# Kernel optimization log

Measured on AMD Instinct MI355X. Metric: run time of the kernel, lower is better.

Reference implementation:

```python
import jax, jax.numpy as jnp
import numpy as np


def _safe_pow(v, p):
    # mimic torch.nan_to_num(pow(v, p), nan=0, posinf=0, neginf=0) for v >= 0
    out = jnp.where(v > 0, jnp.power(jnp.where(v > 0, v, 1.0), p), 0.0)
    return out.astype(jnp.float32)


def setup_inputs() -> dict:
    key = jax.random.key(0)
    k1, k2, k3 = jax.random.split(key, 3)
    N, E, Din, Dout = 20000, 4096, 128, 128
    x = jax.random.normal(k1, (N, Din), dtype=jnp.float32)
    H = jax.random.uniform(k2, (N, E), dtype=jnp.float32)
    W = jax.random.normal(k3, (Dout, Din), dtype=jnp.float32) * (1.0 / np.sqrt(Din))
    b = jnp.zeros((Dout,), dtype=jnp.float32)
    return {"x": x, "H": H, "W": W, "b": b}


def reference(x, H, W, b):
    # Dv^{-1/2}: node degrees; De^{-1}: hyperedge degrees.
    # torch.diag(...)**p with nan/inf->0 is exactly diagonal scaling, so we
    # use broadcasted vector scaling fused around the two GEMMs.
    dv = _safe_pow(jnp.sum(H, axis=-1), -0.5)   # [N]
    de = _safe_pow(jnp.sum(H, axis=0), -1.0)    # [E]
    x = dv[:, None] * x                          # Dv^{-1/2} x
    x = H.T @ x                                  # [E, Din]
    x = de[:, None] * x                          # De^{-1}
    x = H @ x                                    # [N, Din]
    x = dv[:, None] * x                          # Dv^{-1/2}
    return x @ W.T + b                           # Linear
```

## Files before the change

kernel.cpp:

```cpp
#include <hip/hip_runtime.h>
#include <hip/hip_bf16.h>
#include <stdint.h>


#define N_ 20000
#define E_ 4096
#define D_ 128
#define XTB_S 20032
#define SPLIT 12

typedef __attribute__((ext_vector_type(8))) short    bf16x8;
typedef __attribute__((ext_vector_type(4))) float    f32x4;
typedef __attribute__((ext_vector_type(8))) unsigned short us8;
typedef __attribute__((ext_vector_type(4))) unsigned short us4;

__device__ __forceinline__ unsigned short f2bf(float f) {
  unsigned u = __float_as_uint(f);
  u += 0x7FFFu + ((u >> 16) & 1u);
  return (unsigned short)(u >> 16);
}
__device__ __forceinline__ unsigned cvtpk(float lo, float hi) {
  unsigned r;
  asm("v_cvt_pk_bf16_f32 %0, %1, %2" : "=v"(r) : "v"(lo), "v"(hi));
  return r;
}
__device__ __forceinline__ void gload16(const unsigned short* g, unsigned short* l) {
  __builtin_amdgcn_global_load_lds(
      (const __attribute__((address_space(1))) unsigned int*)g,
      (__attribute__((address_space(3))) unsigned int*)l, 16, 0, 0);
}

__global__ __launch_bounds__(256) void k_pre(const float* __restrict__ H,
                                             const float* __restrict__ x,
                                             const float* __restrict__ W,
                                             float* __restrict__ dv,
                                             unsigned short* __restrict__ Hb,
                                             unsigned short* __restrict__ xTb,
                                             unsigned short* __restrict__ Wb) {
  const int t = threadIdx.x, lane = t & 63, w = t >> 6;
  const int b = blockIdx.x;
  if (b >= 2500) {
    const size_t base = (size_t)(20000 + (b - 2500) * 8) * E_;
    for (int i = t; i < 4096; i += 256)
      *(us8*)&Hb[base + (size_t)i * 8] = (us8){0,0,0,0,0,0,0,0};
    if (b == 2500 && t < 128) {
#pragma unroll
      for (int c = 0; c < 4; ++c)
        *(us8*)&xTb[(size_t)t * XTB_S + 20000 + c * 8] = (us8){0,0,0,0,0,0,0,0};
    }
    if (b == 2501) {
      int base2 = t * 64;
#pragma unroll
      for (int i = 0; i < 8; ++i) {
        const float* wp = W + base2 + i * 8;
        f32x4 a = *(const f32x4*)wp, b4 = *(const f32x4*)(wp + 4);
        union { us8 v; unsigned u[4]; } un;
        un.u[0] = cvtpk(a.x, a.y);   un.u[1] = cvtpk(a.z, a.w);
        un.u[2] = cvtpk(b4.x, b4.y); un.u[3] = cvtpk(b4.z, b4.w);
        *(us8*)(Wb + base2 + i * 8) = un.v;
      }
    }
    return;
  }
  __shared__ float red[32];
  __shared__ float xt[8 * 128];
  const int n0 = b * 8;
  { int r = t >> 5, d4 = (t & 31) * 4;
    *(f32x4*)&xt[r * 128 + d4] = *(const f32x4*)(x + (size_t)(n0 + r) * D_ + d4); }
  float rs[8];
#pragma unroll
  for (int r = 0; r < 8; ++r) {
    rs[r] = 0.f;
    const float* rp = H + (size_t)(n0 + r) * E_;
    unsigned short* hp = Hb + (size_t)(n0 + r) * E_;
#pragma unroll
    for (int j = 0; j < 4; ++j) {
      f32x4 v = *(const f32x4*)(rp + j * 1024 + t * 4);
      rs[r] += (v.x + v.y) + (v.z + v.w);
      union { us4 v4; unsigned u32[2]; } un;
      un.u32[0] = cvtpk(v.x, v.y);
      un.u32[1] = cvtpk(v.z, v.w);
      *(us4*)(hp + j * 1024 + t * 4) = un.v4;
    }
  }
#pragma unroll
  for (int r = 0; r < 8; ++r)
#pragma unroll
    for (int off = 32; off; off >>= 1) rs[r] += __shfl_xor(rs[r], off);
  if (lane == 0) {
#pragma unroll
    for (int r = 0; r < 8; ++r) red[w * 8 + r] = rs[r];
  }
  __syncthreads();
  if (t < 8) {
    float s = red[t] + red[8 + t] + red[16 + t] + red[24 + t];
    float d = s > 0.f ? rsqrtf(s) : 0.f;
    dv[n0 + t] = d;
    red[t] = d;
  }
  __syncthreads();
  if (t < 128) {
    int d = t;
    float v[8];
#pragma unroll
    for (int r = 0; r < 8; ++r) v[r] = xt[r * 128 + d] * red[r];
    union { us8 v8; unsigned u32[4]; } un;
#pragma unroll
    for (int j = 0; j < 4; ++j) un.u32[j] = cvtpk(v[2 * j], v[2 * j + 1]);
    *(us8*)(xTb + (size_t)d * XTB_S + n0) = un.v8;
  }
}

__global__ __launch_bounds__(256) void k_gemm1(const unsigned short* __restrict__ Hb,
                                               const unsigned short* __restrict__ xTb,
                                               float* __restrict__ partialT,
                                               float* __restrict__ desumP) {
  __shared__ unsigned short lH[2][64 * 64];
  __shared__ unsigned short lX[2][128 * 64];
  const int t = threadIdx.x, lane = t & 63, w = t >> 6;
  const int eb = blockIdx.x & 63, s = blockIdx.x >> 6;
  const int e0 = eb * 64;
  const int g0 = (s * 313) / SPLIT;
  const int g1 = ((s + 1) * 313) / SPLIT;
  const int lrow = lane >> 3, lslot = lane & 7;
  const int bswz = (lslot ^ lrow) << 3;
  const int wy = w >> 1, wx = w & 1;
  const int ep = t & 31, q = t >> 5;
  const int er0 = 2 * ep, er1 = 2 * ep + 1;
  const int sl0 = (q ^ (er0 & 7)) << 3, sl1 = (q ^ (er1 & 7)) << 3;

  f32x4 acc[4][2];
  f32x4 accC[2];
#pragma unroll
  for (int i = 0; i < 4; ++i)
#pragma unroll
    for (int j = 0; j < 2; ++j) acc[i][j] = (f32x4){0.f, 0.f, 0.f, 0.f};
  accC[0] = (f32x4){0.f, 0.f, 0.f, 0.f};
  accC[1] = (f32x4){0.f, 0.f, 0.f, 0.f};
  bf16x8 ones;
#pragma unroll
  for (int i = 0; i < 8; ++i) ones[i] = (short)0x3F80;

  unsigned hr[8];
  auto LOADH = [&](int g) {
    const unsigned short* p = Hb + (size_t)(g * 64 + q * 8) * E_ + e0 + er0;
#pragma unroll
    for (int j = 0; j < 8; ++j) hr[j] = *(const unsigned*)(p + (size_t)j * E_);
  };
  auto WRITEH = [&](int bufi) {
    union { bf16x8 v; unsigned u[4]; } lo, hi;
#pragma unroll
    for (int p = 0; p < 4; ++p) {
      lo.u[p] = (hr[2 * p] & 0xFFFFu) | (hr[2 * p + 1] << 16);
      hi.u[p] = (hr[2 * p] >> 16) | (hr[2 * p + 1] & 0xFFFF0000u);
    }
    *(bf16x8*)&lH[bufi][er0 * 64 + sl0] = lo.v;
    *(bf16x8*)&lH[bufi][er1 * 64 + sl1] = hi.v;
  };
  auto GLOADX = [&](int g, int bufi) {
#pragma unroll
    for (int i = 0; i < 4; ++i) {
      int c = w * 4 + i;
      gload16(xTb + (size_t)(8 * c + lrow) * XTB_S + g * 64 + bswz,
              &lX[bufi][c * 512]);
    }
  };

  LOADH(g0); GLOADX(g0, 0); WRITEH(0);
  __syncthreads();
  int cur = 0;
  for (int it = g0; it < g1; ++it) {
    bool hn = it + 1 < g1;
    if (hn) { LOADH(it + 1); GLOADX(it + 1, cur ^ 1); }
    const int kg = lane >> 4, fr = lane & 15;
    bf16x8 ax[4][2], bh[2][2];
#pragma unroll
    for (int mi = 0; mi < 4; ++mi) {
      int m = wy * 64 + mi * 16 + fr;
#pragma unroll
      for (int kk = 0; kk < 2; ++kk)
        ax[mi][kk] = *(const bf16x8*)&lX[cur][m * 64 + (((kk * 4 + kg) ^ (m & 7)) << 3)];
    }
#pragma unroll
    for (int ni = 0; ni < 2; ++ni) {
      int n = wx * 32 + ni * 16 + fr;
#pragma unroll
      for (int kk = 0; kk < 2; ++kk)
        bh[ni][kk] = *(const bf16x8*)&lH[cur][n * 64 + (((kk * 4 + kg) ^ (n & 7)) << 3)];
    }
#pragma unroll
    for (int kk = 0; kk < 2; ++kk)
#pragma unroll
      for (int mi = 0; mi < 4; ++mi)
#pragma unroll
        for (int ni = 0; ni < 2; ++ni)
          acc[mi][ni] = __builtin_amdgcn_mfma_f32_16x16x32_bf16(ax[mi][kk], bh[ni][kk], acc[mi][ni], 0, 0, 0);
    if (wy == 0) {
#pragma unroll
      for (int kk = 0; kk < 2; ++kk)
#pragma unroll
        for (int ni = 0; ni < 2; ++ni)
          accC[ni] = __builtin_amdgcn_mfma_f32_16x16x32_bf16(ones, bh[ni][kk], accC[ni], 0, 0, 0);
    }
    if (hn) WRITEH(cur ^ 1);
    __syncthreads();
    cur ^= 1;
  }
  const int kg = lane >> 4, fr = lane & 15;
  if (wy == 0 && kg == 0) {
#pragma unroll
    for (int ni = 0; ni < 2; ++ni)
      desumP[s * E_ + e0 + wx * 32 + ni * 16 + fr] = accC[ni][0];
  }
#pragma unroll
  for (int mi = 0; mi < 4; ++mi)
#pragma unroll
    for (int ni = 0; ni < 2; ++ni)
#pragma unroll
      for (int r = 0; r < 4; ++r) {
        int d = wy * 64 + mi * 16 + kg * 4 + r;
        int e = e0 + wx * 32 + ni * 16 + fr;
        partialT[((size_t)s * 128 + d) * E_ + e] = acc[mi][ni][r];
      }
}

__global__ __launch_bounds__(256) void k_mid(const float* __restrict__ partialT,
                                             const float* __restrict__ desumP,
                                             const unsigned short* __restrict__ Wb,
                                             unsigned short* __restrict__ x3WT) {
  __shared__ unsigned short lW[128 * 136];
  __shared__ unsigned short lE[16 * 132];
  __shared__ float lT[128 * 20];
  const int t = threadIdx.x, lane = t & 63, w = t >> 6;
  const int e0 = blockIdx.x * 16;

  {
    int j = t >> 1, half = (t & 1) * 64;
    const us8* src = (const us8*)(Wb + (size_t)j * 128 + half);
#pragma unroll
    for (int i = 0; i < 8; ++i)
      *(us8*)&lW[j * 136 + half + 8 * i] = src[i];
  }
  {
    const int e = e0 + (t & 15);
    const int d0 = (t >> 4) * 8;
    float des = 0.f;
#pragma unroll
    for (int s = 0; s < SPLIT; ++s) des += desumP[s * E_ + e];
    float dei = des > 0.f ? 1.f / des : 0.f;
    float accp[8];
#pragma unroll
    for (int i = 0; i < 8; ++i) accp[i] = 0.f;
#pragma unroll
    for (int s = 0; s < SPLIT; ++s) {
      const float* p = partialT + ((size_t)s * 128 + d0) * E_ + e;
#pragma unroll
      for (int i = 0; i < 8; ++i) accp[i] += p[(size_t)i * E_];
    }
    union { bf16x8 v; unsigned u[4]; } un;
#pragma unroll
    for (int i = 0; i < 4; ++i)
      un.u[i] = cvtpk(accp[2 * i] * dei, accp[2 * i + 1] * dei);
    *(bf16x8*)&lE[(t & 15) * 132 + d0] = un.v;
  }
  __syncthreads();
  const int kg = lane >> 4, fr = lane & 15;
  f32x4 acc[2];
  acc[0] = (f32x4){0.f, 0.f, 0.f, 0.f};
  acc[1] = (f32x4){0.f, 0.f, 0.f, 0.f};
#pragma unroll
  for (int kk = 0; kk < 4; ++kk) {
    bf16x8 bfrag = *(const bf16x8*)&lE[fr * 132 + (kk * 4 + kg) * 8];
#pragma unroll
    for (int mi = 0; mi < 2; ++mi) {
      int m = w * 32 + mi * 16 + fr;
      bf16x8 afrag = *(const bf16x8*)&lW[m * 136 + (kk * 4 + kg) * 8];
      acc[mi] = __builtin_amdgcn_mfma_f32_16x16x32_bf16(afrag, bfrag, acc[mi], 0, 0, 0);
    }
  }
  __syncthreads();
#pragma unroll
  for (int mi = 0; mi < 2; ++mi)
#pragma unroll
    for (int r = 0; r < 4; ++r)
      lT[(w * 32 + mi * 16 + kg * 4 + r) * 20 + fr] = acc[mi][r];
  __syncthreads();
  {
    int j = t >> 1, eh = (t & 1) * 8;
    float v[8];
#pragma unroll
    for (int i = 0; i < 8; ++i) v[i] = lT[j * 20 + eh + i];
    union { us8 v8; unsigned u[4]; } un;
#pragma unroll
    for (int i = 0; i < 4; ++i) un.u[i] = cvtpk(v[2 * i], v[2 * i + 1]);
    *(us8*)(x3WT + (size_t)j * E_ + e0 + eh) = un.v8;
  }
}

__global__ __launch_bounds__(256) void k_gemm2(const unsigned short* __restrict__ Hb,
                                               const unsigned short* __restrict__ x3WT,
                                               const float* __restrict__ dv,
                                               const float* __restrict__ bias,
                                               float* __restrict__ out) {
  __shared__ unsigned short lA[2][64 * 64];
  __shared__ unsigned short lB[2][128 * 64];
  const int t = threadIdx.x, lane = t & 63, w = t >> 6;
  const int n0b = blockIdx.x * 64;
  const int lrow = lane >> 3, lslot = lane & 7;
  const int bswz = (lslot ^ lrow) << 3;
  const int wy = w >> 1, wx = w & 1;

  auto GLOADA = [&](int g, int bufi) {
#pragma unroll
    for (int i = 0; i < 2; ++i) {
      int c = w * 2 + i;
      gload16(Hb + (size_t)(n0b + 8 * c + lrow) * E_ + g * 64 + bswz,
              &lA[bufi][c * 512]);
    }
  };
  auto GLOADB = [&](int g, int bufi) {
#pragma unroll
    for (int i = 0; i < 4; ++i) {
      int c = w * 4 + i;
      gload16(x3WT + (size_t)(8 * c + lrow) * E_ + g * 64 + bswz,
              &lB[bufi][c * 512]);
    }
  };

  f32x4 acc[2][4];
#pragma unroll
  for (int i = 0; i < 2; ++i)
#pragma unroll
    for (int j = 0; j < 4; ++j) acc[i][j] = (f32x4){0.f, 0.f, 0.f, 0.f};

  GLOADA(0, 0); GLOADB(0, 0);
  __syncthreads();
  int cur = 0;
  for (int it = 0; it < 64; ++it) {
    bool hn = it < 63;
    if (hn) { GLOADA(it + 1, cur ^ 1); GLOADB(it + 1, cur ^ 1); }
    const int kg = lane >> 4, fr = lane & 15;
    bf16x8 af[2][2], bfr[4][2];
#pragma unroll
    for (int mi = 0; mi < 2; ++mi) {
      int m = wy * 32 + mi * 16 + fr;
#pragma unroll
      for (int kk = 0; kk < 2; ++kk)
        af[mi][kk] = *(const bf16x8*)&lA[cur][m * 64 + (((kk * 4 + kg) ^ (m & 7)) << 3)];
    }
#pragma unroll
    for (int ni = 0; ni < 4; ++ni) {
      int d = wx * 64 + ni * 16 + fr;
#pragma unroll
      for (int kk = 0; kk < 2; ++kk)
        bfr[ni][kk] = *(const bf16x8*)&lB[cur][d * 64 + (((kk * 4 + kg) ^ (d & 7)) << 3)];
    }
#pragma unroll
    for (int kk = 0; kk < 2; ++kk)
#pragma unroll
      for (int mi = 0; mi < 2; ++mi)
#pragma unroll
        for (int ni = 0; ni < 4; ++ni)
          acc[mi][ni] = __builtin_amdgcn_mfma_f32_16x16x32_bf16(af[mi][kk], bfr[ni][kk], acc[mi][ni], 0, 0, 0);
    __syncthreads();
    cur ^= 1;
  }
  const int kg = lane >> 4, fr = lane & 15;
#pragma unroll
  for (int mi = 0; mi < 2; ++mi) {
    float dvv[4];
#pragma unroll
    for (int r = 0; r < 4; ++r)
      dvv[r] = dv[min(n0b + wy * 32 + mi * 16 + kg * 4 + r, N_ - 1)];
#pragma unroll
    for (int ni = 0; ni < 4; ++ni) {
      int j2 = wx * 64 + ni * 16 + fr;
      float bb = bias[j2];
#pragma unroll
      for (int r = 0; r < 4; ++r) {
        int n = n0b + wy * 32 + mi * 16 + kg * 4 + r;
        if (n < N_) out[(size_t)n * D_ + j2] = acc[mi][ni][r] * dvv[r] + bb;
      }
    }
  }
}

extern "C" void kernel_launch(void* const* d_in, const int* in_sizes, int n_in,
                              void* d_out, int out_size, void* d_ws, size_t ws_size,
                              hipStream_t stream) {
  const float* x = (const float*)d_in[0];
  const float* H = (const float*)d_in[1];
  const float* W = (const float*)d_in[2];
  const float* b = (const float*)d_in[3];
  float* out = (float*)d_out;
  char* ws = (char*)d_ws;
  float*          desumP   = (float*)(ws);
  float*          dv       = (float*)(ws + 196608);
  unsigned short* Wb       = (unsigned short*)(ws + 276736);
  unsigned short* xTb      = (unsigned short*)(ws + 309504);
  unsigned short* x3WT     = (unsigned short*)(ws + 5437696);
  float*          partialT = (float*)(ws + 6486272);
  unsigned short* Hb       = (unsigned short*)(ws + 31652096);

  k_pre<<<2504, 256, 0, stream>>>(H, x, W, dv, Hb, xTb, Wb);
  k_gemm1<<<768, 256, 0, stream>>>(Hb, xTb, partialT, desumP);
  k_mid<<<256, 256, 0, stream>>>(partialT, desumP, Wb, x3WT);
  k_gemm2<<<313, 256, 0, stream>>>(Hb, x3WT, dv, b, out);
}
```

Baseline: 224.0 us.

## Triple-buffer LDS in both GEMMs with explicit vmcnt waits and reduce split

```diff
diff --git a/kernel.cpp b/kernel.cpp
--- a/kernel.cpp
+++ b/kernel.cpp
@@ -7,7 +7,7 @@
 #define E_ 4096
 #define D_ 128
 #define XTB_S 20032
-#define SPLIT 12
+#define SPLIT 8
 
 typedef __attribute__((ext_vector_type(8))) short    bf16x8;
 typedef __attribute__((ext_vector_type(4))) float    f32x4;
@@ -29,6 +29,9 @@
       (const __attribute__((address_space(1))) unsigned int*)g,
       (__attribute__((address_space(3))) unsigned int*)l, 16, 0, 0);
 }
+#define VMCNT(n) asm volatile("s_waitcnt vmcnt(" #n ")" ::: "memory")
+#define LGKM0()  asm volatile("s_waitcnt lgkmcnt(0)" ::: "memory")
+#define BAR()    do { __builtin_amdgcn_s_barrier(); __builtin_amdgcn_sched_barrier(0); } while (0)
 
 __global__ __launch_bounds__(256) void k_pre(const float* __restrict__ H,
                                              const float* __restrict__ x,
@@ -116,7 +119,7 @@
                                                float* __restrict__ partialT,
                                                float* __restrict__ desumP) {
   __shared__ unsigned short lH[2][64 * 64];
-  __shared__ unsigned short lX[2][128 * 64];
+  __shared__ unsigned short lX[3][128 * 64];
   const int t = threadIdx.x, lane = t & 63, w = t >> 6;
   const int eb = blockIdx.x & 63, s = blockIdx.x >> 6;
   const int e0 = eb * 64;
@@ -166,12 +169,20 @@
     }
   };
 
-  LOADH(g0); GLOADX(g0, 0); WRITEH(0);
-  __syncthreads();
-  int cur = 0;
+  LOADH(g0);
+  GLOADX(g0, 0);
+  GLOADX(g0 + 1, 1);
+  WRITEH(0);
+  VMCNT(4);
+  LGKM0();
+  BAR();
+
+  int cur = 0, curH = 0;
   for (int it = g0; it < g1; ++it) {
-    bool hn = it + 1 < g1;
-    if (hn) { LOADH(it + 1); GLOADX(it + 1, cur ^ 1); }
+    const bool hn = it + 1 < g1;
+    if (hn) LOADH(it + 1);
+    const int tn = (it + 2 < g1) ? it + 2 : g1 - 1;
+    GLOADX(tn, cur == 0 ? 2 : cur - 1);
     const int kg = lane >> 4, fr = lane & 15;
     bf16x8 ax[4][2], bh[2][2];
 #pragma unroll
@@ -186,8 +197,9 @@
       int n = wx * 32 + ni * 16 + fr;
 #pragma unroll
       for (int kk = 0; kk < 2; ++kk)
-        bh[ni][kk] = *(const bf16x8*)&lH[cur][n * 64 + (((kk * 4 + kg) ^ (n & 7)) << 3)];
-    }
+        bh[ni][kk] = *(const bf16x8*)&lH[curH][n * 64 + (((kk * 4 + kg) ^ (n & 7)) << 3)];
+    }
+    __builtin_amdgcn_s_setprio(1);
 #pragma unroll
     for (int kk = 0; kk < 2; ++kk)
 #pragma unroll
@@ -202,9 +214,13 @@
         for (int ni = 0; ni < 2; ++ni)
           accC[ni] = __builtin_amdgcn_mfma_f32_16x16x32_bf16(ones, bh[ni][kk], accC[ni], 0, 0, 0);
     }
-    if (hn) WRITEH(cur ^ 1);
-    __syncthreads();
-    cur ^= 1;
+    __builtin_amdgcn_s_setprio(0);
+    if (hn) WRITEH(curH ^ 1);
+    VMCNT(4);
+    LGKM0();
+    BAR();
+    cur = (cur == 2) ? 0 : cur + 1;
+    curH ^= 1;
   }
   const int kg = lane >> 4, fr = lane & 15;
   if (wy == 0 && kg == 0) {
@@ -302,23 +318,21 @@
                                                const float* __restrict__ dv,
                                                const float* __restrict__ bias,
                                                float* __restrict__ out) {
-  __shared__ unsigned short lA[2][64 * 64];
-  __shared__ unsigned short lB[2][128 * 64];
+  __shared__ unsigned short lA[3][64 * 64];
+  __shared__ unsigned short lB[3][128 * 64];
   const int t = threadIdx.x, lane = t & 63, w = t >> 6;
   const int n0b = blockIdx.x * 64;
   const int lrow = lane >> 3, lslot = lane & 7;
   const int bswz = (lslot ^ lrow) << 3;
   const int wy = w >> 1, wx = w & 1;
 
-  auto GLOADA = [&](int g, int bufi) {
+  auto STAGE = [&](int g, int bufi) {
 #pragma unroll
     for (int i = 0; i < 2; ++i) {
       int c = w * 2 + i;
       gload16(Hb + (size_t)(n0b + 8 * c + lrow) * E_ + g * 64 + bswz,
               &lA[bufi][c * 512]);
     }
-  };
-  auto GLOADB = [&](int g, int bufi) {
 #pragma unroll
     for (int i = 0; i < 4; ++i) {
       int c = w * 4 + i;
@@ -333,12 +347,15 @@
 #pragma unroll
     for (int j = 0; j < 4; ++j) acc[i][j] = (f32x4){0.f, 0.f, 0.f, 0.f};
 
-  GLOADA(0, 0); GLOADB(0, 0);
-  __syncthreads();
+  STAGE(0, 0);
+  STAGE(1, 1);
+  VMCNT(6);
+  BAR();
+
   int cur = 0;
   for (int it = 0; it < 64; ++it) {
-    bool hn = it < 63;
-    if (hn) { GLOADA(it + 1, cur ^ 1); GLOADB(it + 1, cur ^ 1); }
+    const int tn = (it + 2 < 64) ? it + 2 : 63;
+    STAGE(tn, cur == 0 ? 2 : cur - 1);
     const int kg = lane >> 4, fr = lane & 15;
     bf16x8 af[2][2], bfr[4][2];
 #pragma unroll
@@ -355,6 +372,7 @@
       for (int kk = 0; kk < 2; ++kk)
         bfr[ni][kk] = *(const bf16x8*)&lB[cur][d * 64 + (((kk * 4 + kg) ^ (d & 7)) << 3)];
     }
+    __builtin_amdgcn_s_setprio(1);
 #pragma unroll
     for (int kk = 0; kk < 2; ++kk)
 #pragma unroll
@@ -362,8 +380,10 @@
 #pragma unroll
         for (int ni = 0; ni < 4; ++ni)
           acc[mi][ni] = __builtin_amdgcn_mfma_f32_16x16x32_bf16(af[mi][kk], bfr[ni][kk], acc[mi][ni], 0, 0, 0);
-    __syncthreads();
-    cur ^= 1;
+    __builtin_amdgcn_s_setprio(0);
+    VMCNT(6);
+    BAR();
+    cur = (cur == 2) ? 0 : cur + 1;
   }
   const int kg = lane >> 4, fr = lane & 15;
 #pragma unroll
@@ -395,15 +415,15 @@
   float* out = (float*)d_out;
   char* ws = (char*)d_ws;
   float*          desumP   = (float*)(ws);
-  float*          dv       = (float*)(ws + 196608);
-  unsigned short* Wb       = (unsigned short*)(ws + 276736);
-  unsigned short* xTb      = (unsigned short*)(ws + 309504);
-  unsigned short* x3WT     = (unsigned short*)(ws + 5437696);
-  float*          partialT = (float*)(ws + 6486272);
-  unsigned short* Hb       = (unsigned short*)(ws + 31652096);
+  float*          dv       = (float*)(ws + 131072);
+  unsigned short* Wb       = (unsigned short*)(ws + 211200);
+  unsigned short* xTb      = (unsigned short*)(ws + 243968);
+  unsigned short* x3WT     = (unsigned short*)(ws + 5372160);
+  float*          partialT = (float*)(ws + 6420736);
+  unsigned short* Hb       = (unsigned short*)(ws + 23197952);
 
   k_pre<<<2504, 256, 0, stream>>>(H, x, W, dv, Hb, xTb, Wb);
-  k_gemm1<<<768, 256, 0, stream>>>(Hb, xTb, partialT, desumP);
+  k_gemm1<<<512, 256, 0, stream>>>(Hb, xTb, partialT, desumP);
   k_mid<<<256, 256, 0, stream>>>(partialT, desumP, Wb, x3WT);
   k_gemm2<<<313, 256, 0, stream>>>(Hb, x3WT, dv, b, out);
 }
```

Result: no change. 228.3 us (+1.9%).

## Split-K the second GEMM into two halves, add reduction kernel, remap gemm1 blocks

Applied to the files above, without the earlier changes.

```diff
diff --git a/kernel.cpp b/kernel.cpp
--- a/kernel.cpp
+++ b/kernel.cpp
@@ -118,7 +118,8 @@
   __shared__ unsigned short lH[2][64 * 64];
   __shared__ unsigned short lX[2][128 * 64];
   const int t = threadIdx.x, lane = t & 63, w = t >> 6;
-  const int eb = blockIdx.x & 63, s = blockIdx.x >> 6;
+  const int virt = (blockIdx.x & 7) * 96 + (blockIdx.x >> 3);
+  const int eb = virt & 63, s = virt >> 6;
   const int e0 = eb * 64;
   const int g0 = (s * 313) / SPLIT;
   const int g1 = ((s + 1) * 313) / SPLIT;
@@ -299,13 +300,13 @@
 
 __global__ __launch_bounds__(256) void k_gemm2(const unsigned short* __restrict__ Hb,
                                                const unsigned short* __restrict__ x3WT,
-                                               const float* __restrict__ dv,
-                                               const float* __restrict__ bias,
-                                               float* __restrict__ out) {
+                                               float* __restrict__ P) {
   __shared__ unsigned short lA[2][64 * 64];
   __shared__ unsigned short lB[2][128 * 64];
   const int t = threadIdx.x, lane = t & 63, w = t >> 6;
-  const int n0b = blockIdx.x * 64;
+  const int tile = blockIdx.x >> 1, half = blockIdx.x & 1;
+  const int n0b = tile * 64;
+  const int gbase = half * 32;
   const int lrow = lane >> 3, lslot = lane & 7;
   const int bswz = (lslot ^ lrow) << 3;
   const int wy = w >> 1, wx = w & 1;
@@ -333,12 +334,12 @@
 #pragma unroll
     for (int j = 0; j < 4; ++j) acc[i][j] = (f32x4){0.f, 0.f, 0.f, 0.f};
 
-  GLOADA(0, 0); GLOADB(0, 0);
+  GLOADA(gbase, 0); GLOADB(gbase, 0);
   __syncthreads();
   int cur = 0;
-  for (int it = 0; it < 64; ++it) {
-    bool hn = it < 63;
-    if (hn) { GLOADA(it + 1, cur ^ 1); GLOADB(it + 1, cur ^ 1); }
+  for (int it = 0; it < 32; ++it) {
+    bool hn = it < 31;
+    if (hn) { GLOADA(gbase + it + 1, cur ^ 1); GLOADB(gbase + it + 1, cur ^ 1); }
     const int kg = lane >> 4, fr = lane & 15;
     bf16x8 af[2][2], bfr[4][2];
 #pragma unroll
@@ -366,23 +367,38 @@
     cur ^= 1;
   }
   const int kg = lane >> 4, fr = lane & 15;
-#pragma unroll
-  for (int mi = 0; mi < 2; ++mi) {
-    float dvv[4];
-#pragma unroll
-    for (int r = 0; r < 4; ++r)
-      dvv[r] = dv[min(n0b + wy * 32 + mi * 16 + kg * 4 + r, N_ - 1)];
+  float* Ph = P + (size_t)half * N_ * D_;
+#pragma unroll
+  for (int mi = 0; mi < 2; ++mi)
 #pragma unroll
     for (int ni = 0; ni < 4; ++ni) {
       int j2 = wx * 64 + ni * 16 + fr;
-      float bb = bias[j2];
 #pragma unroll
       for (int r = 0; r < 4; ++r) {
         int n = n0b + wy * 32 + mi * 16 + kg * 4 + r;
-        if (n < N_) out[(size_t)n * D_ + j2] = acc[mi][ni][r] * dvv[r] + bb;
+        if (n < N_) Ph[(size_t)n * D_ + j2] = acc[mi][ni][r];
       }
     }
-  }
+}
+
+__global__ __launch_bounds__(256) void k_out(const float* __restrict__ P,
+                                             const float* __restrict__ dv,
+                                             const float* __restrict__ bias,
+                                             float* __restrict__ out) {
+  int tid = blockIdx.x * 256 + threadIdx.x;
+  int n = tid >> 4, jb = (tid & 15) * 8;
+  size_t off = (size_t)n * D_ + jb;
+  f32x4 p0a = *(const f32x4*)(P + off);
+  f32x4 p0b = *(const f32x4*)(P + off + 4);
+  f32x4 p1a = *(const f32x4*)(P + (size_t)N_ * D_ + off);
+  f32x4 p1b = *(const f32x4*)(P + (size_t)N_ * D_ + off + 4);
+  f32x4 ba  = *(const f32x4*)(bias + jb);
+  f32x4 bb  = *(const f32x4*)(bias + jb + 4);
+  float d = dv[n];
+  f32x4 oa = (p0a + p1a) * d + ba;
+  f32x4 ob = (p0b + p1b) * d + bb;
+  *(f32x4*)(out + off)     = oa;
+  *(f32x4*)(out + off + 4) = ob;
 }
 
 extern "C" void kernel_launch(void* const* d_in, const int* in_sizes, int n_in,
@@ -401,9 +417,11 @@
   unsigned short* x3WT     = (unsigned short*)(ws + 5437696);
   float*          partialT = (float*)(ws + 6486272);
   unsigned short* Hb       = (unsigned short*)(ws + 31652096);
+  float*          P        = (float*)(ws + 195754240);
 
   k_pre<<<2504, 256, 0, stream>>>(H, x, W, dv, Hb, xTb, Wb);
   k_gemm1<<<768, 256, 0, stream>>>(Hb, xTb, partialT, desumP);
   k_mid<<<256, 256, 0, stream>>>(partialT, desumP, Wb, x3WT);
-  k_gemm2<<<313, 256, 0, stream>>>(Hb, x3WT, dv, b, out);
-}
+  k_gemm2<<<626, 256, 0, stream>>>(Hb, x3WT, P);
+  k_out<<<1250, 256, 0, stream>>>(P, dv, b, out);
+}
```

New measurement: 213.7 us. 1.05x faster.
